# Kernel optimization log

Measured on AMD Instinct MI355X. Metric: run time of the kernel, lower is better.

## Reference

```python
import jax, jax.numpy as jnp
import numpy as np

B, T, WIN, CIN, H, COUT = 512, 64, 256, 4, 512, 2


def setup_inputs() -> dict:
    key = jax.random.key(0)
    k = jax.random.split(key, 4)
    D = WIN * CIN  # 1024
    s = 0.02
    return {
        "inputs": jax.random.normal(k[0], (B, T, WIN, CIN), dtype=jnp.float32),
        "W_in": jax.random.normal(k[1], (D, 3 * H), dtype=jnp.float32) * s,
        "b_in": jnp.zeros((3 * H,), dtype=jnp.float32),
        "U": jax.random.normal(k[2], (H, 3 * H), dtype=jnp.float32) * s,
        "b_rec": jnp.zeros((3 * H,), dtype=jnp.float32),
        "W2": jax.random.normal(k[3], (2 * H, WIN * COUT), dtype=jnp.float32) * s,
        "b2": jnp.zeros((WIN * COUT,), dtype=jnp.float32),
    }


def _gru_last_state(x, W_in, b_in, U, b_rec):
    # Keras GRU v2 math: reset_after=True, recurrent_activation=sigmoid,
    # activation=relu (as configured). training=False -> no dropout.
    Bm, Tm, _ = x.shape
    Hm = U.shape[0]
    # precompute input projections for all timesteps: [B, T, 3H]
    xg = jnp.einsum("btd,dh->bth", x, W_in) + b_in

    def step(h, xg_t):
        hg = h @ U + b_rec  # recurrent bias applied before reset gate (reset_after)
        xz, xr, xh = jnp.split(xg_t, 3, axis=-1)
        hz, hr, hh = jnp.split(hg, 3, axis=-1)
        z = jax.nn.sigmoid(xz + hz)
        r = jax.nn.sigmoid(xr + hr)
        h_cand = jax.nn.relu(xh + r * hh)
        h_new = z * h + (1.0 - z) * h_cand
        return h_new, None

    h0 = jnp.zeros((Bm, Hm), dtype=x.dtype)
    hT, _ = jax.lax.scan(step, h0, jnp.swapaxes(xg, 0, 1))
    return hT  # [B, H]; with return_sequences=False, output == final_state


def reference(inputs, W_in, b_in, U, b_rec, W2, b2):
    Bm, Tm = inputs.shape[0], inputs.shape[1]
    x = inputs.reshape(Bm, Tm, -1)  # flatten window*channels -> [B, T, 1024]
    hT = _gru_last_state(x, W_in, b_in, U, b_rec)
    cat = jnp.concatenate([hT, hT], axis=-1)  # tf.concat((output, final_state))
    out = cat @ W2 + b2
    return out.reshape(Bm, WIN, COUT)
```

## Files before the change

### kernel.cpp

```cpp
#include <hip/hip_runtime.h>
#include <hip/hip_bf16.h>
#include <stdint.h>

#define BATCH 512
#define TSTEPS 64
#define DIN 1024
#define HID 512
#define G3 1536
#define MROWS (BATCH * TSTEPS)
#define POUT 512

typedef __attribute__((ext_vector_type(8))) short bf16x8;
typedef __attribute__((ext_vector_type(4))) float f32x4;

__device__ __forceinline__ float bf2f(short s) {
  union { unsigned u; float f; } v;
  v.u = ((unsigned)(unsigned short)s) << 16;
  return v.f;
}
__device__ __forceinline__ short f2bf(float f) {
  __hip_bfloat16 h = __float2bfloat16(f);
  short s;
  __builtin_memcpy(&s, &h, 2);
  return s;
}
__device__ __forceinline__ void gload_lds16(const void* g, void* l) {
  __builtin_amdgcn_global_load_lds(
      (const __attribute__((address_space(1))) void*)g,
      (__attribute__((address_space(3))) void*)l, 16, 0, 0);
}

__global__ __launch_bounds__(256) void transpose_cast(const float* __restrict__ in,
                                                      short* __restrict__ out,
                                                      int R, int C) {
  __shared__ float tile[32][33];
  const int c0 = blockIdx.x * 32, r0 = blockIdx.y * 32;
  const int tx = threadIdx.x & 31, ty = threadIdx.x >> 5;
#pragma unroll
  for (int i = 0; i < 4; ++i) {
    const int r = r0 + ty + i * 8;
    tile[ty + i * 8][tx] = in[(size_t)r * C + c0 + tx];
  }
  __syncthreads();
#pragma unroll
  for (int i = 0; i < 4; ++i) {
    const int c = c0 + ty + i * 8;
    out[(size_t)c * R + r0 + tx] = f2bf(tile[tx][ty + i * 8]);
  }
}

__global__ __launch_bounds__(256) void u_pack2(const float* __restrict__ U,
                                               short* __restrict__ Upk) {
  const unsigned idx = blockIdx.x * 256 + threadIdx.x;
  const unsigned cg = idx / 49152u;
  const unsigned rem = idx - cg * 49152u;
  const unsigned ur = rem >> 9;
  const unsigned r2 = rem & 511u;
  const unsigned s = r2 >> 3, e = r2 & 7u;
  const unsigned chunk = s ^ (ur & 7u);
  const unsigned k = chunk * 8u + e;
  const unsigned g = ur >> 5, cc = ur & 31u;
  const unsigned col = g * 512u + cg * 32u + cc;
  Upk[idx] = f2bf(U[(size_t)k * G3 + col]);
}

__global__ __launch_bounds__(256) void gemm_xg_mfma(const float* __restrict__ X,
                                                    const short* __restrict__ Wt,
                                                    const float* __restrict__ bin,
                                                    __hip_bfloat16* __restrict__ XG) {
  __shared__ __align__(16) short As[128 * 64];
  __shared__ __align__(16) short Bs[128 * 64];
  const int tid = threadIdx.x;
  const int w = tid >> 6, l = tid & 63;
  const int lc = l & 15, lg = l >> 4;

  const int xcd = blockIdx.x & 7;
  const int idx = blockIdx.x >> 3;
  const int wg = xcd * 384 + idx;
  const int rt = wg / 12, ct = wg % 12;
  const int row0 = rt * 128, col0 = ct * 128;

  const int wm = w >> 1, wn = w & 1;

  f32x4 acc[4][4];
#pragma unroll
  for (int mt = 0; mt < 4; ++mt)
#pragma unroll
    for (int nt = 0; nt < 4; ++nt) acc[mt][nt] = (f32x4){0.f, 0.f, 0.f, 0.f};

  const int tr = tid >> 3, p = tid & 7;

  for (int k0 = 0; k0 < DIN; k0 += 64) {
    float4 ar[4][2];
#pragma unroll
    for (int i = 0; i < 4; ++i) {
      const int r = i * 32 + tr;
      const int s = p ^ (r & 7);
      const float* xp = &X[(size_t)(row0 + r) * DIN + k0 + s * 8];
      ar[i][0] = *reinterpret_cast<const float4*>(xp);
      ar[i][1] = *reinterpret_cast<const float4*>(xp + 4);
    }
    __syncthreads();
#pragma unroll
    for (int i = 0; i < 4; ++i) {
      const int r = i * 32 + tr;
      bf16x8 v;
      v[0] = f2bf(ar[i][0].x); v[1] = f2bf(ar[i][0].y);
      v[2] = f2bf(ar[i][0].z); v[3] = f2bf(ar[i][0].w);
      v[4] = f2bf(ar[i][1].x); v[5] = f2bf(ar[i][1].y);
      v[6] = f2bf(ar[i][1].z); v[7] = f2bf(ar[i][1].w);
      *reinterpret_cast<bf16x8*>((char*)As + r * 128 + p * 16) = v;
    }
#pragma unroll
    for (int i = 0; i < 4; ++i) {
      const int rr = w * 32 + i * 8 + (l >> 3);
      const int pp = l & 7;
      const int s = pp ^ (rr & 7);
      gload_lds16(&Wt[(size_t)(col0 + rr) * DIN + k0 + s * 8],
                  (char*)Bs + (w * 32 + i * 8) * 128);
    }
    __syncthreads();
#pragma unroll
    for (int kc = 0; kc < 2; ++kc) {
      bf16x8 a[4], b[4];
#pragma unroll
      for (int mt = 0; mt < 4; ++mt) {
        const int R = wm * 64 + mt * 16 + lc;
        const int ch = (kc * 4 + lg) ^ (R & 7);
        a[mt] = *reinterpret_cast<const bf16x8*>((const char*)As + R * 128 + ch * 16);
      }
#pragma unroll
      for (int nt = 0; nt < 4; ++nt) {
        const int Rn = wn * 64 + nt * 16 + lc;
        const int ch = (kc * 4 + lg) ^ (Rn & 7);
        b[nt] = *reinterpret_cast<const bf16x8*>((const char*)Bs + Rn * 128 + ch * 16);
      }
#pragma unroll
      for (int mt = 0; mt < 4; ++mt)
#pragma unroll
        for (int nt = 0; nt < 4; ++nt)
          acc[mt][nt] = __builtin_amdgcn_mfma_f32_16x16x32_bf16(a[mt], b[nt],
                                                                acc[mt][nt], 0, 0, 0);
    }
  }

  float bv[4];
#pragma unroll
  for (int nt = 0; nt < 4; ++nt) bv[nt] = bin[col0 + wn * 64 + nt * 16 + lc];
#pragma unroll
  for (int mt = 0; mt < 4; ++mt) {
#pragma unroll
    for (int nt = 0; nt < 4; ++nt) {
      const int col = col0 + wn * 64 + nt * 16 + lc;
#pragma unroll
      for (int rr = 0; rr < 4; ++rr) {
        const int m = row0 + wm * 64 + mt * 16 + lg * 4 + rr;
        const size_t rowp = (size_t)(m & 63) * 512 + (m >> 6);
        XG[rowp * G3 + col] = __float2bfloat16(acc[mt][nt][rr] + bv[nt]);
      }
    }
  }
}

__global__ __launch_bounds__(256) void gru_scan_coop(
    const __hip_bfloat16* __restrict__ XG, const short* __restrict__ Upk,
    const float* __restrict__ brec, short* h_g, unsigned* bar,
    float* __restrict__ HT) {
  __shared__ __align__(16) short Us[96 * 512];
  __shared__ __align__(16) short hS[32 * 512];
  __shared__ __align__(16) short xgL[2][3072];
  const int tid = threadIdx.x, w = tid >> 6, l = tid & 63;
  const int lc = l & 15, lg = l >> 4;
  const int bg = blockIdx.x >> 4, cgi = blockIdx.x & 15;
  const int b0 = bg * 32, c0 = cgi * 32;
  const int wm = w >> 1, wn = w & 1;

  {
    const short* usrc = Upk + (size_t)cgi * 49152;
#pragma unroll
    for (int r = 0; r < 24; ++r)
      gload_lds16(usrc + (r * 256 + tid) * 8, Us + (r * 256 + (tid & ~63)) * 8);
  }
  for (int i = tid; i < 4096; i += 256) ((unsigned long long*)hS)[i] = 0ull;

  const int i0 = tid;
  const int bl0 = i0 / 12, q0 = i0 - bl0 * 12;
  const int off0 = bl0 * 1536 + (q0 >> 2) * 512 + c0 + (q0 & 3) * 8;
  const int i1 = 256 + tid;
  const int bl1 = i1 / 12, q1 = i1 - bl1 * 12;
  const int off1 = bl1 * 1536 + (q1 >> 2) * 512 + c0 + (q1 & 3) * 8;

  const short* XGs = (const short*)XG;
  {
    const short* xs = XGs + (size_t)b0 * 1536;
    gload_lds16(xs + off0, (char*)xgL + w * 1024);
    if (tid < 128) gload_lds16(xs + off1, (char*)xgL + 4096 + w * 1024);
  }

  const int j = c0 + wn * 16 + lc;
  const float brz = brec[j], brr = brec[512 + j], brh = brec[1024 + j];
  const int arow = wm * 16 + lc;
  const int ur0 = wn * 16 + lc;

  __syncthreads();

  for (int t = 0; t < TSTEPS; ++t) {
    if (t > 0) {
      const unsigned long long* hsrc = (const unsigned long long*)(
          h_g + ((size_t)(t & 1) * BATCH + b0) * 512);
      unsigned long long v[16];
#pragma unroll
      for (int r = 0; r < 16; ++r)
        v[r] = __hip_atomic_load(hsrc + r * 256 + tid, __ATOMIC_RELAXED,
                                 __HIP_MEMORY_SCOPE_AGENT);
#pragma unroll
      for (int r = 0; r < 16; ++r)
        ((unsigned long long*)hS)[r * 256 + tid] = v[r];
      __syncthreads();
    }

    f32x4 za0 = (f32x4){0.f, 0.f, 0.f, 0.f}, za1 = za0, za2 = za0;
#pragma unroll
    for (int kc = 0; kc < 16; ++kc) {
      const int s = kc * 4 + lg;
      const bf16x8 a = *(const bf16x8*)((const char*)hS + arow * 1024 +
                                        (s ^ (arow & 7)) * 16);
      const char* ub =
          (const char*)Us + ur0 * 1024 + (s ^ (ur0 & 7)) * 16;
      const bf16x8 bz = *(const bf16x8*)(ub);
      const bf16x8 brg = *(const bf16x8*)(ub + 32 * 1024);
      const bf16x8 bh = *(const bf16x8*)(ub + 64 * 1024);
      za0 = __builtin_amdgcn_mfma_f32_16x16x32_bf16(a, bz, za0, 0, 0, 0);
      za1 = __builtin_amdgcn_mfma_f32_16x16x32_bf16(a, brg, za1, 0, 0, 0);
      za2 = __builtin_amdgcn_mfma_f32_16x16x32_bf16(a, bh, za2, 0, 0, 0);
    }

    const short* xb = xgL[t & 1];
#pragma unroll
    for (int r = 0; r < 4; ++r) {
      const int lb = wm * 16 + lg * 4 + r;
      const float xz = bf2f(xb[lb * 96 + wn * 16 + lc]);
      const float xr = bf2f(xb[lb * 96 + 32 + wn * 16 + lc]);
      const float xh = bf2f(xb[lb * 96 + 64 + wn * 16 + lc]);
      const float z = 1.f / (1.f + __expf(-(xz + za0[r] + brz)));
      const float rg = 1.f / (1.f + __expf(-(xr + za1[r] + brr)));
      const float hc = fmaxf(fmaf(rg, za2[r] + brh, xh), 0.f);
      const int hoff = lb * 1024 + (((j >> 3) ^ (lb & 7)) << 4) + (j & 7) * 2;
      const float hold = bf2f(*(const short*)((const char*)hS + hoff));
      const float hnew = fmaf(z, hold - hc, hc);
      if (t == TSTEPS - 1) {
        HT[(size_t)(b0 + lb) * HID + j] = hnew;
      } else {
        __hip_atomic_store(
            (unsigned short*)((char*)h_g +
                              ((size_t)((t + 1) & 1) * BATCH + b0) * 1024 + hoff),
            (unsigned short)f2bf(hnew), __ATOMIC_RELAXED,
            __HIP_MEMORY_SCOPE_AGENT);
      }
    }
    if (t == TSTEPS - 1) break;

    __syncthreads();
    if (tid == 0)
      __hip_atomic_store(&bar[bg * 16 + cgi], (unsigned)(t + 1),
                         __ATOMIC_RELAXED, __HIP_MEMORY_SCOPE_AGENT);
    {
      const short* xs = XGs + ((size_t)(t + 1) * 512 + b0) * 1536;
      char* xd = (char*)xgL + ((t + 1) & 1) * 6144;
      gload_lds16(xs + off0, xd + w * 1024);
      if (tid < 128) gload_lds16(xs + off1, xd + 4096 + w * 1024);
    }
    if (w == 0 && l < 16) {
      while (__hip_atomic_load(&bar[bg * 16 + l], __ATOMIC_RELAXED,
                               __HIP_MEMORY_SCOPE_AGENT) < (unsigned)(t + 1))
        __builtin_amdgcn_s_sleep(1);
    }
    __syncthreads();
  }
}

__global__ __launch_bounds__(256) void final_proj(const float* __restrict__ HT,
                                                  const float* __restrict__ W2,
                                                  const float* __restrict__ b2,
                                                  float* __restrict__ OUT) {
  const int b = blockIdx.x >> 1;
  const int pp = ((blockIdx.x & 1) << 8) + threadIdx.x;
  float acc = b2[pp];
  const float* h = &HT[(size_t)b * HID];
  for (int k = 0; k < HID; ++k)
    acc = fmaf(h[k], W2[(size_t)k * POUT + pp] + W2[(size_t)(k + HID) * POUT + pp], acc);
  OUT[(size_t)b * POUT + pp] = acc;
}

extern "C" void kernel_launch(void* const* d_in, const int* in_sizes, int n_in,
                              void* d_out, int out_size, void* d_ws,
                              size_t ws_size, hipStream_t stream) {
  const float* X    = (const float*)d_in[0];
  const float* Win  = (const float*)d_in[1];
  const float* bin  = (const float*)d_in[2];
  const float* U    = (const float*)d_in[3];
  const float* brec = (const float*)d_in[4];
  const float* W2   = (const float*)d_in[5];
  const float* b2   = (const float*)d_in[6];
  float* OUT = (float*)d_out;

  char* ws = (char*)d_ws;
  size_t off = 0;
  __hip_bfloat16* XG = (__hip_bfloat16*)(ws + off); off += (size_t)MROWS * G3 * 2;
  short* Wt   = (short*)(ws + off); off += (size_t)G3 * DIN * 2;
  short* Upk  = (short*)(ws + off); off += (size_t)G3 * HID * 2;
  float* HT   = (float*)(ws + off); off += (size_t)BATCH * HID * 4;
  short* h_g  = (short*)(ws + off); off += (size_t)2 * BATCH * HID * 2;
  unsigned* bar = (unsigned*)(ws + off);

  hipMemsetAsync(bar, 0, 1024, stream);

  transpose_cast<<<dim3(G3 / 32, DIN / 32), 256, 0, stream>>>(Win, Wt, DIN, G3);
  u_pack2<<<(16 * 96 * 512) / 256, 256, 0, stream>>>(U, Upk);
  gemm_xg_mfma<<<(MROWS / 128) * (G3 / 128), 256, 0, stream>>>(X, Wt, bin, XG);

  const __hip_bfloat16* XGc = XG;
  const short* Upkc = Upk;
  void* args[] = {(void*)&XGc, (void*)&Upkc, (void*)&brec,
                  (void*)&h_g, (void*)&bar, (void*)&HT};
  hipLaunchCooperativeKernel((const void*)gru_scan_coop, dim3(256), dim3(256),
                             args, 0, stream);

  final_proj<<<(BATCH * POUT) / 256, 256, 0, stream>>>(HT, W2, b2, OUT);
}
```

Measured before the change: 473.8 us.

## Load recurrent state directly into MFMA registers and spin per-wave on flags

Removes the shared-memory staging buffer for the hidden state. Each wave now polls the group's 16 completion flags itself, then loads its own h rows straight from global memory into MFMA operand registers. The previous block-wide spin by wave 0 and the extra __syncthreads per step are gone, and the old h value is kept in registers instead of being re-read. This cuts LDS traffic and barrier latency on the serial critical path, but each wave now does redundant global loads and polling, and the h layout in global memory loses its swizzle.

```diff
diff --git a/kernel.cpp b/kernel.cpp
--- a/kernel.cpp
+++ b/kernel.cpp
@@ -167,13 +167,13 @@
     const float* __restrict__ brec, short* h_g, unsigned* bar,
     float* __restrict__ HT) {
   __shared__ __align__(16) short Us[96 * 512];
-  __shared__ __align__(16) short hS[32 * 512];
   __shared__ __align__(16) short xgL[2][3072];
   const int tid = threadIdx.x, w = tid >> 6, l = tid & 63;
   const int lc = l & 15, lg = l >> 4;
   const int bg = blockIdx.x >> 4, cgi = blockIdx.x & 15;
   const int b0 = bg * 32, c0 = cgi * 32;
   const int wm = w >> 1, wn = w & 1;
+  unsigned* const flags = bar + bg * 16;
 
   {
     const short* usrc = Upk + (size_t)cgi * 49152;
@@ -181,7 +181,6 @@
     for (int r = 0; r < 24; ++r)
       gload_lds16(usrc + (r * 256 + tid) * 8, Us + (r * 256 + (tid & ~63)) * 8);
   }
-  for (int i = tid; i < 4096; i += 256) ((unsigned long long*)hS)[i] = 0ull;
 
   const int i0 = tid;
   const int bl0 = i0 / 12, q0 = i0 - bl0 * 12;
@@ -199,40 +198,46 @@
 
   const int j = c0 + wn * 16 + lc;
   const float brz = brec[j], brr = brec[512 + j], brh = brec[1024 + j];
-  const int arow = wm * 16 + lc;
   const int ur0 = wn * 16 + lc;
+  float hold[4] = {0.f, 0.f, 0.f, 0.f};
 
   __syncthreads();
 
   for (int t = 0; t < TSTEPS; ++t) {
+    f32x4 za0 = (f32x4){0.f, 0.f, 0.f, 0.f}, za1 = za0, za2 = za0;
     if (t > 0) {
-      const unsigned long long* hsrc = (const unsigned long long*)(
-          h_g + ((size_t)(t & 1) * BATCH + b0) * 512);
-      unsigned long long v[16];
-#pragma unroll
-      for (int r = 0; r < 16; ++r)
-        v[r] = __hip_atomic_load(hsrc + r * 256 + tid, __ATOMIC_RELAXED,
-                                 __HIP_MEMORY_SCOPE_AGENT);
-#pragma unroll
-      for (int r = 0; r < 16; ++r)
-        ((unsigned long long*)hS)[r * 256 + tid] = v[r];
-      __syncthreads();
-    }
-
-    f32x4 za0 = (f32x4){0.f, 0.f, 0.f, 0.f}, za1 = za0, za2 = za0;
-#pragma unroll
-    for (int kc = 0; kc < 16; ++kc) {
-      const int s = kc * 4 + lg;
-      const bf16x8 a = *(const bf16x8*)((const char*)hS + arow * 1024 +
-                                        (s ^ (arow & 7)) * 16);
-      const char* ub =
-          (const char*)Us + ur0 * 1024 + (s ^ (ur0 & 7)) * 16;
-      const bf16x8 bz = *(const bf16x8*)(ub);
-      const bf16x8 brg = *(const bf16x8*)(ub + 32 * 1024);
-      const bf16x8 bh = *(const bf16x8*)(ub + 64 * 1024);
-      za0 = __builtin_amdgcn_mfma_f32_16x16x32_bf16(a, bz, za0, 0, 0, 0);
-      za1 = __builtin_amdgcn_mfma_f32_16x16x32_bf16(a, brg, za1, 0, 0, 0);
-      za2 = __builtin_amdgcn_mfma_f32_16x16x32_bf16(a, bh, za2, 0, 0, 0);
+      for (;;) {
+        const unsigned f = __hip_atomic_load(&flags[l & 15], __ATOMIC_RELAXED,
+                                             __HIP_MEMORY_SCOPE_AGENT);
+        if (__all((int)(f >= (unsigned)t))) break;
+        __builtin_amdgcn_s_sleep(1);
+      }
+      const unsigned long long* hrow = (const unsigned long long*)(
+          h_g + ((size_t)(t & 1) * BATCH + b0 + wm * 16 + lc) * 512);
+      unsigned long long va[32];
+#pragma unroll
+      for (int kc = 0; kc < 16; ++kc) {
+        va[2 * kc] = __hip_atomic_load(hrow + kc * 8 + lg * 2,
+                                       __ATOMIC_RELAXED,
+                                       __HIP_MEMORY_SCOPE_AGENT);
+        va[2 * kc + 1] = __hip_atomic_load(hrow + kc * 8 + lg * 2 + 1,
+                                           __ATOMIC_RELAXED,
+                                           __HIP_MEMORY_SCOPE_AGENT);
+      }
+#pragma unroll
+      for (int kc = 0; kc < 16; ++kc) {
+        union { unsigned long long q[2]; bf16x8 v; } ua;
+        ua.q[0] = va[2 * kc];
+        ua.q[1] = va[2 * kc + 1];
+        const char* ub = (const char*)Us + ur0 * 1024 +
+                         (((kc * 4 + lg) ^ (ur0 & 7)) << 4);
+        const bf16x8 bz = *(const bf16x8*)(ub);
+        const bf16x8 brg = *(const bf16x8*)(ub + 32 * 1024);
+        const bf16x8 bh = *(const bf16x8*)(ub + 64 * 1024);
+        za0 = __builtin_amdgcn_mfma_f32_16x16x32_bf16(ua.v, bz, za0, 0, 0, 0);
+        za1 = __builtin_amdgcn_mfma_f32_16x16x32_bf16(ua.v, brg, za1, 0, 0, 0);
+        za2 = __builtin_amdgcn_mfma_f32_16x16x32_bf16(ua.v, bh, za2, 0, 0, 0);
+      }
     }
 
     const short* xb = xgL[t & 1];
@@ -245,15 +250,13 @@
       const float z = 1.f / (1.f + __expf(-(xz + za0[r] + brz)));
       const float rg = 1.f / (1.f + __expf(-(xr + za1[r] + brr)));
       const float hc = fmaxf(fmaf(rg, za2[r] + brh, xh), 0.f);
-      const int hoff = lb * 1024 + (((j >> 3) ^ (lb & 7)) << 4) + (j & 7) * 2;
-      const float hold = bf2f(*(const short*)((const char*)hS + hoff));
-      const float hnew = fmaf(z, hold - hc, hc);
+      const float hnew = fmaf(z, hold[r] - hc, hc);
+      hold[r] = hnew;
       if (t == TSTEPS - 1) {
         HT[(size_t)(b0 + lb) * HID + j] = hnew;
       } else {
         __hip_atomic_store(
-            (unsigned short*)((char*)h_g +
-                              ((size_t)((t + 1) & 1) * BATCH + b0) * 1024 + hoff),
+            (unsigned short*)(h_g + ((size_t)((t + 1) & 1) * BATCH + b0 + lb) * 512 + j),
             (unsigned short)f2bf(hnew), __ATOMIC_RELAXED,
             __HIP_MEMORY_SCOPE_AGENT);
       }
@@ -262,20 +265,14 @@
 
     __syncthreads();
     if (tid == 0)
-      __hip_atomic_store(&bar[bg * 16 + cgi], (unsigned)(t + 1),
-                         __ATOMIC_RELAXED, __HIP_MEMORY_SCOPE_AGENT);
+      __hip_atomic_store(&flags[cgi], (unsigned)(t + 1), __ATOMIC_RELAXED,
+                         __HIP_MEMORY_SCOPE_AGENT);
     {
       const short* xs = XGs + ((size_t)(t + 1) * 512 + b0) * 1536;
       char* xd = (char*)xgL + ((t + 1) & 1) * 6144;
       gload_lds16(xs + off0, xd + w * 1024);
       if (tid < 128) gload_lds16(xs + off1, xd + 4096 + w * 1024);
     }
-    if (w == 0 && l < 16) {
-      while (__hip_atomic_load(&bar[bg * 16 + l], __ATOMIC_RELAXED,
-                               __HIP_MEMORY_SCOPE_AGENT) < (unsigned)(t + 1))
-        __builtin_amdgcn_s_sleep(1);
-    }
-    __syncthreads();
   }
 }
 
```

Result: slower. 656.5 us (+38.5%).

## Tile XG per scan block and replace end-of-step barrier with per-wave flag polling

Applied to the files above, without the earlier changes.

The input-projection GEMM now writes XG in a block-tiled layout so each scan block's per-step slice (32 batch rows × 96 gate columns) is contiguous, making the prefetch a simple linear copy. The inter-block barrier is restructured: instead of one wave spinning and then a block-wide __syncthreads, every wave polls the 16 group flags with a wave-wide vote at the start of the next step, which removes one __syncthreads per step. The first-step MFMA is skipped because h is zero. The risk is extra polling traffic from all waves, and the correctness of the memory ordering now depends on each wave observing the flags itself.

```diff
diff --git a/kernel.cpp b/kernel.cpp
--- a/kernel.cpp
+++ b/kernel.cpp
@@ -152,11 +152,15 @@
 #pragma unroll
     for (int nt = 0; nt < 4; ++nt) {
       const int col = col0 + wn * 64 + nt * 16 + lc;
+      const int g = col >> 9, cgc = (col >> 5) & 15, cc = col & 31;
 #pragma unroll
       for (int rr = 0; rr < 4; ++rr) {
         const int m = row0 + wm * 64 + mt * 16 + lg * 4 + rr;
-        const size_t rowp = (size_t)(m & 63) * 512 + (m >> 6);
-        XG[rowp * G3 + col] = __float2bfloat16(acc[mt][nt][rr] + bv[nt]);
+        const int t = m & 63, b = m >> 6;
+        const size_t o =
+            ((((size_t)t * 16 + (b >> 5)) * 16 + cgc) * 32 + (b & 31)) * 96 +
+            g * 32 + cc;
+        XG[o] = __float2bfloat16(acc[mt][nt][rr] + bv[nt]);
       }
     }
   }
@@ -174,6 +178,7 @@
   const int bg = blockIdx.x >> 4, cgi = blockIdx.x & 15;
   const int b0 = bg * 32, c0 = cgi * 32;
   const int wm = w >> 1, wn = w & 1;
+  unsigned* const flags = bar + bg * 16;
 
   {
     const short* usrc = Upk + (size_t)cgi * 49152;
@@ -183,18 +188,12 @@
   }
   for (int i = tid; i < 4096; i += 256) ((unsigned long long*)hS)[i] = 0ull;
 
-  const int i0 = tid;
-  const int bl0 = i0 / 12, q0 = i0 - bl0 * 12;
-  const int off0 = bl0 * 1536 + (q0 >> 2) * 512 + c0 + (q0 & 3) * 8;
-  const int i1 = 256 + tid;
-  const int bl1 = i1 / 12, q1 = i1 - bl1 * 12;
-  const int off1 = bl1 * 1536 + (q1 >> 2) * 512 + c0 + (q1 & 3) * 8;
-
   const short* XGs = (const short*)XG;
   {
-    const short* xs = XGs + (size_t)b0 * 1536;
-    gload_lds16(xs + off0, (char*)xgL + w * 1024);
-    if (tid < 128) gload_lds16(xs + off1, (char*)xgL + 4096 + w * 1024);
+    const short* xs = XGs + (size_t)bg * 49152 + (size_t)cgi * 3072;
+    gload_lds16(xs + tid * 8, (char*)xgL[0] + w * 1024);
+    if (tid < 128)
+      gload_lds16(xs + (256 + tid) * 8, (char*)xgL[0] + 4096 + w * 1024);
   }
 
   const int j = c0 + wn * 16 + lc;
@@ -205,7 +204,14 @@
   __syncthreads();
 
   for (int t = 0; t < TSTEPS; ++t) {
+    f32x4 za0 = (f32x4){0.f, 0.f, 0.f, 0.f}, za1 = za0, za2 = za0;
     if (t > 0) {
+      for (;;) {
+        const unsigned f = __hip_atomic_load(&flags[l & 15], __ATOMIC_RELAXED,
+                                             __HIP_MEMORY_SCOPE_AGENT);
+        if (__all((int)(f >= (unsigned)t))) break;
+        __builtin_amdgcn_s_sleep(1);
+      }
       const unsigned long long* hsrc = (const unsigned long long*)(
           h_g + ((size_t)(t & 1) * BATCH + b0) * 512);
       unsigned long long v[16];
@@ -217,22 +223,20 @@
       for (int r = 0; r < 16; ++r)
         ((unsigned long long*)hS)[r * 256 + tid] = v[r];
       __syncthreads();
-    }
-
-    f32x4 za0 = (f32x4){0.f, 0.f, 0.f, 0.f}, za1 = za0, za2 = za0;
-#pragma unroll
-    for (int kc = 0; kc < 16; ++kc) {
-      const int s = kc * 4 + lg;
-      const bf16x8 a = *(const bf16x8*)((const char*)hS + arow * 1024 +
-                                        (s ^ (arow & 7)) * 16);
-      const char* ub =
-          (const char*)Us + ur0 * 1024 + (s ^ (ur0 & 7)) * 16;
-      const bf16x8 bz = *(const bf16x8*)(ub);
-      const bf16x8 brg = *(const bf16x8*)(ub + 32 * 1024);
-      const bf16x8 bh = *(const bf16x8*)(ub + 64 * 1024);
-      za0 = __builtin_amdgcn_mfma_f32_16x16x32_bf16(a, bz, za0, 0, 0, 0);
-      za1 = __builtin_amdgcn_mfma_f32_16x16x32_bf16(a, brg, za1, 0, 0, 0);
-      za2 = __builtin_amdgcn_mfma_f32_16x16x32_bf16(a, bh, za2, 0, 0, 0);
+
+#pragma unroll
+      for (int kc = 0; kc < 16; ++kc) {
+        const int s = kc * 4 + lg;
+        const bf16x8 a = *(const bf16x8*)((const char*)hS + arow * 1024 +
+                                          ((s ^ (arow & 7)) << 4));
+        const char* ub = (const char*)Us + ur0 * 1024 + ((s ^ (ur0 & 7)) << 4);
+        const bf16x8 bz = *(const bf16x8*)(ub);
+        const bf16x8 brg = *(const bf16x8*)(ub + 32 * 1024);
+        const bf16x8 bh = *(const bf16x8*)(ub + 64 * 1024);
+        za0 = __builtin_amdgcn_mfma_f32_16x16x32_bf16(a, bz, za0, 0, 0, 0);
+        za1 = __builtin_amdgcn_mfma_f32_16x16x32_bf16(a, brg, za1, 0, 0, 0);
+        za2 = __builtin_amdgcn_mfma_f32_16x16x32_bf16(a, bh, za2, 0, 0, 0);
+      }
     }
 
     const short* xb = xgL[t & 1];
@@ -262,20 +266,16 @@
 
     __syncthreads();
     if (tid == 0)
-      __hip_atomic_store(&bar[bg * 16 + cgi], (unsigned)(t + 1),
-                         __ATOMIC_RELAXED, __HIP_MEMORY_SCOPE_AGENT);
+      __hip_atomic_store(&flags[cgi], (unsigned)(t + 1), __ATOMIC_RELAXED,
+                         __HIP_MEMORY_SCOPE_AGENT);
     {
-      const short* xs = XGs + ((size_t)(t + 1) * 512 + b0) * 1536;
-      char* xd = (char*)xgL + ((t + 1) & 1) * 6144;
-      gload_lds16(xs + off0, xd + w * 1024);
-      if (tid < 128) gload_lds16(xs + off1, xd + 4096 + w * 1024);
-    }
-    if (w == 0 && l < 16) {
-      while (__hip_atomic_load(&bar[bg * 16 + l], __ATOMIC_RELAXED,
-                               __HIP_MEMORY_SCOPE_AGENT) < (unsigned)(t + 1))
-        __builtin_amdgcn_s_sleep(1);
-    }
-    __syncthreads();
+      const short* xs = XGs + ((size_t)(t + 1) * 16 + (size_t)bg) * 49152 +
+                        (size_t)cgi * 3072;
+      char* xd = (char*)xgL[(t + 1) & 1];
+      gload_lds16(xs + tid * 8, xd + w * 1024);
+      if (tid < 128)
+        gload_lds16(xs + (256 + tid) * 8, xd + 4096 + w * 1024);
+    }
   }
 }
 
```

After: 485.5 us. +2.5%, slower.
